# Kernel optimization log

Measured on AMD Instinct MI355X. Metric: run time of the kernel, lower is better.

The kernel has to match this reference:

```python
import jax, jax.numpy as jnp
import numpy as np

NODE_DIM = 64  # Net.node_dim


def _peg_conv(x, pos, edge_index, W, b, em_w, em_b):
    """PEGConv: GCN norm (with self-loops) + positional edge gate sigmoid(Linear(1,1)(sqdist))."""
    n = x.shape[0]
    loop = jnp.arange(n)
    row = jnp.concatenate([edge_index[0], loop])  # source j (with self-loops)
    col = jnp.concatenate([edge_index[1], loop])  # target i
    ones = jnp.ones(row.shape[0], dtype=x.dtype)
    deg = jax.ops.segment_sum(ones, col, num_segments=n)
    dinv = jnp.where(deg > 0, jax.lax.rsqrt(deg), 0.0)
    norm = dinv[row] * dinv[col]                                       # [E+N]
    h = x @ W                                                          # [N, out]
    sq = jnp.sum((pos[col] - pos[row]) ** 2, axis=-1, keepdims=True)   # [E+N, 1]
    gate = jax.nn.sigmoid(sq * em_w[0, 0] + em_b[0])                   # edge MLP Linear(1,1)+Sigmoid
    msg = gate * (norm[:, None] * h[row])                              # [E+N, out]
    return jax.ops.segment_sum(msg, col, num_segments=n) + b


def setup_inputs() -> dict:
    key = jax.random.key(0)
    ks = jax.random.split(key, 12)
    N, E_MP, E_LP = 50000, 800000, 100000
    IN, POS, HID = 128, 32, 64
    return {
        "x": jax.random.normal(ks[0], (N, IN), jnp.float32),
        "pos": jax.random.normal(ks[1], (N, POS), jnp.float32),
        "pos_edge_index": jax.random.randint(ks[2], (2, E_LP), 0, N),
        "neg_edge_index": jax.random.randint(ks[3], (2, E_LP), 0, N),
        "train_pos": jax.random.randint(ks[4], (2, E_MP), 0, N),
        "W1": jax.random.normal(ks[5], (IN, HID), jnp.float32) / np.float32(np.sqrt(IN)),
        "b1": jnp.zeros((HID,), jnp.float32),
        "em1_w": jax.random.normal(ks[6], (1, 1), jnp.float32),
        "em1_b": jnp.zeros((1,), jnp.float32),
        "W2": jax.random.normal(ks[7], (HID, HID), jnp.float32) / np.float32(np.sqrt(HID)),
        "b2": jnp.zeros((HID,), jnp.float32),
        "em2_w": jax.random.normal(ks[8], (1, 1), jnp.float32),
        "em2_b": jnp.zeros((1,), jnp.float32),
        "fc_w": jax.random.normal(ks[9], (1, 2), jnp.float32),  # nn.Linear(2,1) weight
        "fc_b": jnp.zeros((1,), jnp.float32),
    }


def reference(x, pos, pos_edge_index, neg_edge_index, train_pos,
              W1, b1, em1_w, em1_b, W2, b2, em2_w, em2_b, fc_w, fc_b):
    edge_index = jnp.concatenate([pos_edge_index, neg_edge_index], axis=-1)  # [2, 2*E_LP]
    h = _peg_conv(x, pos, train_pos, W1, b1, em1_w, em1_b)
    h = _peg_conv(h, pos, train_pos, W2, b2, em2_w, em2_b)
    nodes_first = h[edge_index[0], :NODE_DIM]
    nodes_second = h[edge_index[1], :NODE_DIM]
    pe = jnp.sum((pos[edge_index[0]] - pos[edge_index[1]]) ** 2, axis=-1, keepdims=True)
    pred = jnp.sum(nodes_first * nodes_second, axis=-1, keepdims=True)
    feats = jnp.concatenate([pred, pe], axis=1)  # [2*E_LP, 2]
    return feats @ fc_w.T + fc_b                 # [2*E_LP, 1]
```

## Files before the change

kernel.cpp:

```cpp
#include <hip/hip_runtime.h>

#define HID 64
#define POS_DIM 32
#define IN_DIM 128

using short8 = __attribute__((ext_vector_type(8))) short;
using f32x4  = __attribute__((ext_vector_type(4))) float;

__device__ __forceinline__ float fsig(float v) {
    return 1.0f / (1.0f + __expf(-v));
}

__device__ __forceinline__ unsigned short f2bf(float f) {
    unsigned int u = __float_as_uint(f);
    u = u + 0x7FFFu + ((u >> 16) & 1u);
    return (unsigned short)(u >> 16);
}
__device__ __forceinline__ float bf2f(unsigned short s) {
    return __uint_as_float(((unsigned int)s) << 16);
}
__device__ __forceinline__ float2 bfpair(unsigned int u) {
    return make_float2(__uint_as_float(u << 16),
                       __uint_as_float(u & 0xFFFF0000u));
}
__device__ __forceinline__ unsigned int pack2bf(float a, float b) {
    return (unsigned int)f2bf(a) | ((unsigned int)f2bf(b) << 16);
}

__global__ __launch_bounds__(256) void k_pre(const int* __restrict__ tp,
                                             const float* __restrict__ pos,
                                             int* cnt, float* __restrict__ sq,
                                             int* __restrict__ rank, int E) {
    int lane = threadIdx.x & 63;
    int wid  = threadIdx.x >> 6;
    int sub  = lane >> 3;
    int j    = lane & 7;
    int e = (blockIdx.x * 4 + wid) * 8 + sub;
    if (e >= E) return;
    int row = tp[e];
    int col = tp[E + e];
    float4 a = ((const float4*)(pos + (size_t)row * POS_DIM))[j];
    float4 b = ((const float4*)(pos + (size_t)col * POS_DIM))[j];
    float dx = a.x - b.x, dy = a.y - b.y, dz = a.z - b.z, dw = a.w - b.w;
    float s = 0.0f;
    s = fmaf(dx, dx, s); s = fmaf(dy, dy, s);
    s = fmaf(dz, dz, s); s = fmaf(dw, dw, s);
    s += __shfl_xor(s, 1);
    s += __shfl_xor(s, 2);
    s += __shfl_xor(s, 4);
    if (j == 0) {
        sq[e] = s;
        rank[e] = atomicAdd(&cnt[col], 1);
    }
}

__global__ __launch_bounds__(256) void k_bsum(const int* __restrict__ cnt,
                                              int* __restrict__ bsum, int n) {
    int i = blockIdx.x * 256 + threadIdx.x;
    int v = (i < n) ? cnt[i] : 0;
    #pragma unroll
    for (int o = 32; o; o >>= 1) v += __shfl_down(v, o);
    __shared__ int w[4];
    int lane = threadIdx.x & 63, wid = threadIdx.x >> 6;
    if (lane == 0) w[wid] = v;
    __syncthreads();
    if (threadIdx.x == 0) bsum[blockIdx.x] = w[0] + w[1] + w[2] + w[3];
}

__global__ __launch_bounds__(256) void k_scan2(const int* __restrict__ cnt,
                                               const int* __restrict__ bsum,
                                               int* __restrict__ off,
                                               float* __restrict__ dinv,
                                               int n, int Etot) {
    __shared__ int s[256];
    __shared__ int wsum[4];
    int tid = threadIdx.x, bid = blockIdx.x;
    int p = 0;
    for (int t = tid; t < bid; t += 256) p += bsum[t];
    #pragma unroll
    for (int o = 32; o; o >>= 1) p += __shfl_down(p, o);
    int lane = tid & 63, wid = tid >> 6;
    if (lane == 0) wsum[wid] = p;
    __syncthreads();
    int bpre = wsum[0] + wsum[1] + wsum[2] + wsum[3];
    int i = bid * 256 + tid;
    int v = (i < n) ? cnt[i] : 0;
    s[tid] = v;
    __syncthreads();
    #pragma unroll
    for (int d = 1; d < 256; d <<= 1) {
        int t_ = (tid >= d) ? s[tid - d] : 0;
        __syncthreads();
        s[tid] += t_;
        __syncthreads();
    }
    if (i < n) {
        off[i]  = bpre + s[tid] - v;
        dinv[i] = rsqrtf((float)(v + 1));
    }
    if (i == 0) off[n] = Etot;
}

__global__ __launch_bounds__(256) void k_fill(const int* __restrict__ tp,
                                              const int* __restrict__ off,
                                              const int* __restrict__ rank,
                                              const float* __restrict__ sq,
                                              const float* __restrict__ dinv,
                                              const float* em1w, const float* em1b,
                                              const float* em2w, const float* em2b,
                                              int4* __restrict__ csr, int E) {
    int e = blockIdx.x * blockDim.x + threadIdx.x;
    if (e >= E) return;
    int row = tp[e];
    int col = tp[E + e];
    int slot = off[col] + rank[e];
    float nrm = dinv[row] * dinv[col];
    float s = sq[e];
    float c1 = fsig(s * em1w[0] + em1b[0]) * nrm;
    float c2 = fsig(s * em2w[0] + em2b[0]) * nrm;
    csr[slot] = make_int4(row, __float_as_int(c1), __float_as_int(c2), 0);
}

template<int K, bool IN_BF16>
__global__ __launch_bounds__(256) void k_gemm_mfma(const void* __restrict__ Xv,
                                                   const float* __restrict__ W,
                                                   unsigned short* __restrict__ H,
                                                   int n) {
    constexpr int RB   = K * 2;
    constexpr int CPR  = K / 8;
    __shared__ unsigned char lds[64 * RB * 2];
    unsigned char* As = lds;
    unsigned char* Bt = lds + 64 * RB;

    int tid  = threadIdx.x;
    int row0 = blockIdx.x * 64;

    for (int i = tid; i < 64 * CPR; i += 256) {
        int r  = i / CPR;
        int kb = i % CPR;
        uint4 val;
        if (row0 + r < n) {
            if (IN_BF16) {
                val = *(const uint4*)((const unsigned short*)Xv + (size_t)(row0 + r) * K + kb * 8);
            } else {
                const float* src = (const float*)Xv + (size_t)(row0 + r) * K + kb * 8;
                float4 f0 = ((const float4*)src)[0];
                float4 f1 = ((const float4*)src)[1];
                val.x = pack2bf(f0.x, f0.y); val.y = pack2bf(f0.z, f0.w);
                val.z = pack2bf(f1.x, f1.y); val.w = pack2bf(f1.z, f1.w);
            }
        } else {
            val = make_uint4(0, 0, 0, 0);
        }
        *(uint4*)(As + r * RB + ((kb ^ (r & 7)) << 4)) = val;
    }
    for (int i = tid; i < K * 16; i += 256) {
        int k  = i / 16;
        int c0 = (i % 16) * 4;
        float4 w = ((const float4*)W)[i];
        #pragma unroll
        for (int u = 0; u < 4; ++u) {
            int c = c0 + u;
            float vv = (u == 0) ? w.x : (u == 1) ? w.y : (u == 2) ? w.z : w.w;
            int byte = c * RB + ((((k * 2) >> 4) ^ (c & 7)) << 4) + ((k & 7) * 2);
            *(unsigned short*)(Bt + byte) = f2bf(vv);
        }
    }
    __syncthreads();

    int wv   = tid >> 6;
    int lane = tid & 63;
    int l15  = lane & 15;
    int g    = lane >> 4;

    f32x4 acc[4] = {{0,0,0,0},{0,0,0,0},{0,0,0,0},{0,0,0,0}};
    #pragma unroll
    for (int kk = 0; kk < K / 32; ++kk) {
        int kc = kk * 4 + g;
        int arow = wv * 16 + l15;
        short8 a = *(const short8*)(As + arow * RB + ((kc ^ (arow & 7)) << 4));
        #pragma unroll
        for (int cb = 0; cb < 4; ++cb) {
            int c = cb * 16 + l15;
            short8 b = *(const short8*)(Bt + c * RB + ((kc ^ (c & 7)) << 4));
            acc[cb] = __builtin_amdgcn_mfma_f32_16x16x32_bf16(a, b, acc[cb], 0, 0, 0);
        }
    }

    #pragma unroll
    for (int cb = 0; cb < 4; ++cb) {
        #pragma unroll
        for (int r = 0; r < 4; ++r) {
            int row = row0 + wv * 16 + g * 4 + r;
            if (row < n) H[(size_t)row * HID + cb * 16 + l15] = f2bf(acc[cb][r]);
        }
    }
}

template<bool BF16OUT>
__global__ __launch_bounds__(256) void k_agg(const int* __restrict__ off,
                                             const int4* __restrict__ csr,
                                             const unsigned short* __restrict__ h,
                                             const float* __restrict__ dinv,
                                             const float* __restrict__ bias,
                                             const float* emb,
                                             void* __restrict__ outv, int n,
                                             int layer) {
    int wid  = threadIdx.x >> 6;
    int lane = threadIdx.x & 63;
    int i = blockIdx.x * 4 + wid;
    if (i >= n) return;
    float di = dinv[i];
    float gself = fsig(emb[0]);
    float acc = bias[lane] + gself * di * di * bf2f(h[(size_t)i * HID + lane]);
    int s = off[i], s1 = off[i + 1];
    for (; s + 4 <= s1; s += 4) {
        int4 e0 = csr[s],     e1 = csr[s + 1];
        int4 e2 = csr[s + 2], e3 = csr[s + 3];
        float c0 = __int_as_float(layer ? e0.z : e0.y);
        float c1 = __int_as_float(layer ? e1.z : e1.y);
        float c2 = __int_as_float(layer ? e2.z : e2.y);
        float c3 = __int_as_float(layer ? e3.z : e3.y);
        float v0 = bf2f(h[(size_t)e0.x * HID + lane]);
        float v1 = bf2f(h[(size_t)e1.x * HID + lane]);
        float v2 = bf2f(h[(size_t)e2.x * HID + lane]);
        float v3 = bf2f(h[(size_t)e3.x * HID + lane]);
        acc = fmaf(c0, v0, acc); acc = fmaf(c1, v1, acc);
        acc = fmaf(c2, v2, acc); acc = fmaf(c3, v3, acc);
    }
    for (; s < s1; ++s) {
        int4 e0 = csr[s];
        acc = fmaf(__int_as_float(layer ? e0.z : e0.y),
                   bf2f(h[(size_t)e0.x * HID + lane]), acc);
    }
    if (BF16OUT) ((unsigned short*)outv)[(size_t)i * HID + lane] = f2bf(acc);
    else         ((float*)outv)[(size_t)i * HID + lane] = acc;
}

__global__ __launch_bounds__(256) void k_predict(const int* __restrict__ pei,
                                                 const int* __restrict__ nei,
                                                 const unsigned short* __restrict__ h,
                                                 const float* __restrict__ pos,
                                                 const float* fcw, const float* fcb,
                                                 float* __restrict__ out, int Elp) {
    int j = threadIdx.x & 7;
    int e = blockIdx.x * 32 + (threadIdx.x >> 3);
    if (e >= 2 * Elp) return;
    int src, dst;
    if (e < Elp) { src = pei[e];        dst = pei[Elp + e]; }
    else         { src = nei[e - Elp];  dst = nei[e];       }
    uint4 hs = ((const uint4*)(h + (size_t)src * HID))[j];
    uint4 hd = ((const uint4*)(h + (size_t)dst * HID))[j];
    float p = 0.0f;
    {
        float2 a, b;
        a = bfpair(hs.x); b = bfpair(hd.x);
        p = fmaf(a.x, b.x, p); p = fmaf(a.y, b.y, p);
        a = bfpair(hs.y); b = bfpair(hd.y);
        p = fmaf(a.x, b.x, p); p = fmaf(a.y, b.y, p);
        a = bfpair(hs.z); b = bfpair(hd.z);
        p = fmaf(a.x, b.x, p); p = fmaf(a.y, b.y, p);
        a = bfpair(hs.w); b = bfpair(hd.w);
        p = fmaf(a.x, b.x, p); p = fmaf(a.y, b.y, p);
    }
    float4 pa = ((const float4*)(pos + (size_t)src * POS_DIM))[j];
    float4 pb = ((const float4*)(pos + (size_t)dst * POS_DIM))[j];
    float dx = pa.x - pb.x, dy = pa.y - pb.y, dz = pa.z - pb.z, dw = pa.w - pb.w;
    float pe = 0.0f;
    pe = fmaf(dx, dx, pe); pe = fmaf(dy, dy, pe);
    pe = fmaf(dz, dz, pe); pe = fmaf(dw, dw, pe);
    p  += __shfl_xor(p, 1);  pe += __shfl_xor(pe, 1);
    p  += __shfl_xor(p, 2);  pe += __shfl_xor(pe, 2);
    p  += __shfl_xor(p, 4);  pe += __shfl_xor(pe, 4);
    if (j == 0) out[e] = fcw[0] * p + fcw[1] * pe + fcb[0];
}

static inline size_t align16(size_t v) { return (v + 15) & ~(size_t)15; }

extern "C" void kernel_launch(void* const* d_in, const int* in_sizes, int n_in,
                              void* d_out, int out_size, void* d_ws, size_t ws_size,
                              hipStream_t stream) {
    const float* x    = (const float*)d_in[0];
    const float* pos  = (const float*)d_in[1];
    const int*   pei  = (const int*)d_in[2];
    const int*   nei  = (const int*)d_in[3];
    const int*   tp   = (const int*)d_in[4];
    const float* W1   = (const float*)d_in[5];
    const float* b1   = (const float*)d_in[6];
    const float* em1w = (const float*)d_in[7];
    const float* em1b = (const float*)d_in[8];
    const float* W2   = (const float*)d_in[9];
    const float* b2   = (const float*)d_in[10];
    const float* em2w = (const float*)d_in[11];
    const float* em2b = (const float*)d_in[12];
    const float* fcw  = (const float*)d_in[13];
    const float* fcb  = (const float*)d_in[14];
    float* outp = (float*)d_out;

    const int N   = in_sizes[0] / IN_DIM;
    const int E   = in_sizes[4] / 2;
    const int Elp = in_sizes[2] / 2;
    const int NB  = (N + 255) / 256;

    char* base = (char*)d_ws;
    size_t o = 0;
    int4* csr = (int4*)(base + o);          o += align16((size_t)E * 16);
    int*   cnt  = (int*)(base + o);         o += align16((size_t)N * 4);
    int*   off  = (int*)(base + o);         o += align16((size_t)(N + 1) * 4);
    int*   bsum = (int*)(base + o);         o += align16((size_t)NB * 4);
    float* dinv = (float*)(base + o);       o += align16((size_t)N * 4);
    unsigned short* obuf = (unsigned short*)(base + o); o += align16((size_t)N * HID * 4);
    char*  region = base + o;
    int*   rank = (int*)region;
    float* sq   = (float*)(region + align16((size_t)E * 4));
    unsigned short* hbuf = (unsigned short*)region;

    hipMemsetAsync(cnt, 0, (size_t)N * 4, stream);
    k_pre<<<(E + 31) / 32, 256, 0, stream>>>(tp, pos, cnt, sq, rank, E);
    k_bsum<<<NB, 256, 0, stream>>>(cnt, bsum, N);
    k_scan2<<<NB, 256, 0, stream>>>(cnt, bsum, off, dinv, N, E);
    k_fill<<<(E + 255) / 256, 256, 0, stream>>>(tp, off, rank, sq, dinv,
                                                em1w, em1b, em2w, em2b, csr, E);

    k_gemm_mfma<IN_DIM, false><<<(N + 63) / 64, 256, 0, stream>>>(x, W1, hbuf, N);
    k_agg<true><<<(N + 3) / 4, 256, 0, stream>>>(off, csr, hbuf, dinv, b1, em1b,
                                                 (void*)obuf, N, 0);

    k_gemm_mfma<HID, true><<<(N + 63) / 64, 256, 0, stream>>>(obuf, W2, hbuf, N);
    k_agg<true><<<(N + 3) / 4, 256, 0, stream>>>(off, csr, hbuf, dinv, b2, em2b,
                                                 (void*)obuf, N, 1);

    k_predict<<<(2 * Elp + 31) / 32, 256, 0, stream>>>(pei, nei, obuf,
                                                       pos, fcw, fcb, outp, Elp);
}
```

Baseline: 189.9 us.

## Restructure CSR build with cursor atomics and split aggregation across half-waves

The CSR build now runs a plain histogram kernel, then the scan also writes a per-node cursor array. A fused fill kernel computes the squared distance, gates and slot (via atomicAdd on the cursor) in one pass, which removes the rank and sq intermediate arrays and their extra global traffic. The aggregation kernel now has each half-wave process alternate edges, loading two packed bf16 features per lane, and combines the halves with a shuffle. This doubles edge-level parallelism per wavefront. The CSR order within a row becomes nondeterministic, so the float summation order varies between runs.

```diff
diff --git a/kernel.cpp b/kernel.cpp
--- a/kernel.cpp
+++ b/kernel.cpp
@@ -27,10 +27,69 @@
     return (unsigned int)f2bf(a) | ((unsigned int)f2bf(b) << 16);
 }
 
-__global__ __launch_bounds__(256) void k_pre(const int* __restrict__ tp,
-                                             const float* __restrict__ pos,
-                                             int* cnt, float* __restrict__ sq,
-                                             int* __restrict__ rank, int E) {
+__global__ __launch_bounds__(256) void k_hist(const int* __restrict__ tp,
+                                              int* cnt, int E) {
+    int i = blockIdx.x * blockDim.x + threadIdx.x;
+    if (i < E) atomicAdd(&cnt[tp[E + i]], 1);
+}
+
+__global__ __launch_bounds__(256) void k_bsum(const int* __restrict__ cnt,
+                                              int* __restrict__ bsum, int n) {
+    int i = blockIdx.x * 256 + threadIdx.x;
+    int v = (i < n) ? cnt[i] : 0;
+    #pragma unroll
+    for (int o = 32; o; o >>= 1) v += __shfl_down(v, o);
+    __shared__ int w[4];
+    int lane = threadIdx.x & 63, wid = threadIdx.x >> 6;
+    if (lane == 0) w[wid] = v;
+    __syncthreads();
+    if (threadIdx.x == 0) bsum[blockIdx.x] = w[0] + w[1] + w[2] + w[3];
+}
+
+__global__ __launch_bounds__(256) void k_scan2(const int* __restrict__ cnt,
+                                               const int* __restrict__ bsum,
+                                               int* __restrict__ off,
+                                               int* __restrict__ cur,
+                                               float* __restrict__ dinv,
+                                               int n, int Etot) {
+    __shared__ int s[256];
+    __shared__ int wsum[4];
+    int tid = threadIdx.x, bid = blockIdx.x;
+    int p = 0;
+    for (int t = tid; t < bid; t += 256) p += bsum[t];
+    #pragma unroll
+    for (int o = 32; o; o >>= 1) p += __shfl_down(p, o);
+    int lane = tid & 63, wid = tid >> 6;
+    if (lane == 0) wsum[wid] = p;
+    __syncthreads();
+    int bpre = wsum[0] + wsum[1] + wsum[2] + wsum[3];
+    int i = bid * 256 + tid;
+    int v = (i < n) ? cnt[i] : 0;
+    s[tid] = v;
+    __syncthreads();
+    #pragma unroll
+    for (int d = 1; d < 256; d <<= 1) {
+        int t_ = (tid >= d) ? s[tid - d] : 0;
+        __syncthreads();
+        s[tid] += t_;
+        __syncthreads();
+    }
+    if (i < n) {
+        int ov = bpre + s[tid] - v;
+        off[i]  = ov;
+        cur[i]  = ov;
+        dinv[i] = rsqrtf((float)(v + 1));
+    }
+    if (i == 0) off[n] = Etot;
+}
+
+__global__ __launch_bounds__(256) void k_fill2(const int* __restrict__ tp,
+                                               const float* __restrict__ pos,
+                                               const float* __restrict__ dinv,
+                                               int* cur,
+                                               const float* em1w, const float* em1b,
+                                               const float* em2w, const float* em2b,
+                                               int4* __restrict__ csr, int E) {
     int lane = threadIdx.x & 63;
     int wid  = threadIdx.x >> 6;
     int sub  = lane >> 3;
@@ -49,76 +108,12 @@
     s += __shfl_xor(s, 2);
     s += __shfl_xor(s, 4);
     if (j == 0) {
-        sq[e] = s;
-        rank[e] = atomicAdd(&cnt[col], 1);
-    }
-}
-
-__global__ __launch_bounds__(256) void k_bsum(const int* __restrict__ cnt,
-                                              int* __restrict__ bsum, int n) {
-    int i = blockIdx.x * 256 + threadIdx.x;
-    int v = (i < n) ? cnt[i] : 0;
-    #pragma unroll
-    for (int o = 32; o; o >>= 1) v += __shfl_down(v, o);
-    __shared__ int w[4];
-    int lane = threadIdx.x & 63, wid = threadIdx.x >> 6;
-    if (lane == 0) w[wid] = v;
-    __syncthreads();
-    if (threadIdx.x == 0) bsum[blockIdx.x] = w[0] + w[1] + w[2] + w[3];
-}
-
-__global__ __launch_bounds__(256) void k_scan2(const int* __restrict__ cnt,
-                                               const int* __restrict__ bsum,
-                                               int* __restrict__ off,
-                                               float* __restrict__ dinv,
-                                               int n, int Etot) {
-    __shared__ int s[256];
-    __shared__ int wsum[4];
-    int tid = threadIdx.x, bid = blockIdx.x;
-    int p = 0;
-    for (int t = tid; t < bid; t += 256) p += bsum[t];
-    #pragma unroll
-    for (int o = 32; o; o >>= 1) p += __shfl_down(p, o);
-    int lane = tid & 63, wid = tid >> 6;
-    if (lane == 0) wsum[wid] = p;
-    __syncthreads();
-    int bpre = wsum[0] + wsum[1] + wsum[2] + wsum[3];
-    int i = bid * 256 + tid;
-    int v = (i < n) ? cnt[i] : 0;
-    s[tid] = v;
-    __syncthreads();
-    #pragma unroll
-    for (int d = 1; d < 256; d <<= 1) {
-        int t_ = (tid >= d) ? s[tid - d] : 0;
-        __syncthreads();
-        s[tid] += t_;
-        __syncthreads();
-    }
-    if (i < n) {
-        off[i]  = bpre + s[tid] - v;
-        dinv[i] = rsqrtf((float)(v + 1));
-    }
-    if (i == 0) off[n] = Etot;
-}
-
-__global__ __launch_bounds__(256) void k_fill(const int* __restrict__ tp,
-                                              const int* __restrict__ off,
-                                              const int* __restrict__ rank,
-                                              const float* __restrict__ sq,
-                                              const float* __restrict__ dinv,
-                                              const float* em1w, const float* em1b,
-                                              const float* em2w, const float* em2b,
-                                              int4* __restrict__ csr, int E) {
-    int e = blockIdx.x * blockDim.x + threadIdx.x;
-    if (e >= E) return;
-    int row = tp[e];
-    int col = tp[E + e];
-    int slot = off[col] + rank[e];
-    float nrm = dinv[row] * dinv[col];
-    float s = sq[e];
-    float c1 = fsig(s * em1w[0] + em1b[0]) * nrm;
-    float c2 = fsig(s * em2w[0] + em2b[0]) * nrm;
-    csr[slot] = make_int4(row, __float_as_int(c1), __float_as_int(c2), 0);
+        float nrm = dinv[row] * dinv[col];
+        float c1 = fsig(s * em1w[0] + em1b[0]) * nrm;
+        float c2 = fsig(s * em2w[0] + em2b[0]) * nrm;
+        int slot = atomicAdd(&cur[col], 1);
+        csr[slot] = make_int4(row, __float_as_int(c1), __float_as_int(c2), 0);
+    }
 }
 
 template<int K, bool IN_BF16>
@@ -197,44 +192,51 @@
     }
 }
 
-template<bool BF16OUT>
 __global__ __launch_bounds__(256) void k_agg(const int* __restrict__ off,
                                              const int4* __restrict__ csr,
                                              const unsigned short* __restrict__ h,
                                              const float* __restrict__ dinv,
                                              const float* __restrict__ bias,
                                              const float* emb,
-                                             void* __restrict__ outv, int n,
-                                             int layer) {
+                                             unsigned short* __restrict__ out,
+                                             int n, int layer) {
     int wid  = threadIdx.x >> 6;
     int lane = threadIdx.x & 63;
+    int half = lane >> 5;
+    int q    = lane & 31;
     int i = blockIdx.x * 4 + wid;
     if (i >= n) return;
-    float di = dinv[i];
-    float gself = fsig(emb[0]);
-    float acc = bias[lane] + gself * di * di * bf2f(h[(size_t)i * HID + lane]);
-    int s = off[i], s1 = off[i + 1];
-    for (; s + 4 <= s1; s += 4) {
-        int4 e0 = csr[s],     e1 = csr[s + 1];
-        int4 e2 = csr[s + 2], e3 = csr[s + 3];
-        float c0 = __int_as_float(layer ? e0.z : e0.y);
-        float c1 = __int_as_float(layer ? e1.z : e1.y);
-        float c2 = __int_as_float(layer ? e2.z : e2.y);
-        float c3 = __int_as_float(layer ? e3.z : e3.y);
-        float v0 = bf2f(h[(size_t)e0.x * HID + lane]);
-        float v1 = bf2f(h[(size_t)e1.x * HID + lane]);
-        float v2 = bf2f(h[(size_t)e2.x * HID + lane]);
-        float v3 = bf2f(h[(size_t)e3.x * HID + lane]);
-        acc = fmaf(c0, v0, acc); acc = fmaf(c1, v1, acc);
-        acc = fmaf(c2, v2, acc); acc = fmaf(c3, v3, acc);
-    }
-    for (; s < s1; ++s) {
-        int4 e0 = csr[s];
-        acc = fmaf(__int_as_float(layer ? e0.z : e0.y),
-                   bf2f(h[(size_t)e0.x * HID + lane]), acc);
-    }
-    if (BF16OUT) ((unsigned short*)outv)[(size_t)i * HID + lane] = f2bf(acc);
-    else         ((float*)outv)[(size_t)i * HID + lane] = acc;
+    float accx = 0.0f, accy = 0.0f;
+    if (half == 0) {
+        float di = dinv[i];
+        float sc = fsig(emb[0]) * di * di;
+        float2 bv = ((const float2*)bias)[q];
+        float2 hv = bfpair(((const unsigned int*)(h + (size_t)i * HID))[q]);
+        accx = fmaf(sc, hv.x, bv.x);
+        accy = fmaf(sc, hv.y, bv.y);
+    }
+    int s  = off[i] + half;
+    int s1 = off[i + 1];
+    for (; s + 2 < s1; s += 4) {
+        int4 ea = csr[s];
+        int4 eb = csr[s + 2];
+        float ca = __int_as_float(layer ? ea.z : ea.y);
+        float cb = __int_as_float(layer ? eb.z : eb.y);
+        float2 va = bfpair(((const unsigned int*)(h + (size_t)ea.x * HID))[q]);
+        float2 vb = bfpair(((const unsigned int*)(h + (size_t)eb.x * HID))[q]);
+        accx = fmaf(ca, va.x, accx); accy = fmaf(ca, va.y, accy);
+        accx = fmaf(cb, vb.x, accx); accy = fmaf(cb, vb.y, accy);
+    }
+    if (s < s1) {
+        int4 ea = csr[s];
+        float ca = __int_as_float(layer ? ea.z : ea.y);
+        float2 va = bfpair(((const unsigned int*)(h + (size_t)ea.x * HID))[q]);
+        accx = fmaf(ca, va.x, accx); accy = fmaf(ca, va.y, accy);
+    }
+    accx += __shfl_down(accx, 32);
+    accy += __shfl_down(accy, 32);
+    if (half == 0)
+        ((unsigned int*)out)[(size_t)i * (HID / 2) + q] = pack2bf(accx, accy);
 }
 
 __global__ __launch_bounds__(256) void k_predict(const int* __restrict__ pei,
@@ -304,31 +306,27 @@
 
     char* base = (char*)d_ws;
     size_t o = 0;
-    int4* csr = (int4*)(base + o);          o += align16((size_t)E * 16);
-    int*   cnt  = (int*)(base + o);         o += align16((size_t)N * 4);
-    int*   off  = (int*)(base + o);         o += align16((size_t)(N + 1) * 4);
-    int*   bsum = (int*)(base + o);         o += align16((size_t)NB * 4);
-    float* dinv = (float*)(base + o);       o += align16((size_t)N * 4);
-    unsigned short* obuf = (unsigned short*)(base + o); o += align16((size_t)N * HID * 4);
-    char*  region = base + o;
-    int*   rank = (int*)region;
-    float* sq   = (float*)(region + align16((size_t)E * 4));
-    unsigned short* hbuf = (unsigned short*)region;
+    int4* csr = (int4*)(base + o);                        o += align16((size_t)E * 16);
+    int*   cnt  = (int*)(base + o);                       o += align16((size_t)N * 4);
+    int*   off  = (int*)(base + o);                       o += align16((size_t)(N + 1) * 4);
+    int*   cur  = (int*)(base + o);                       o += align16((size_t)N * 4);
+    int*   bsum = (int*)(base + o);                       o += align16((size_t)NB * 4);
+    float* dinv = (float*)(base + o);                     o += align16((size_t)N * 4);
+    unsigned short* hbuf = (unsigned short*)(base + o);   o += align16((size_t)N * HID * 2);
+    unsigned short* obuf = (unsigned short*)(base + o);   o += align16((size_t)N * HID * 2);
 
     hipMemsetAsync(cnt, 0, (size_t)N * 4, stream);
-    k_pre<<<(E + 31) / 32, 256, 0, stream>>>(tp, pos, cnt, sq, rank, E);
+    k_hist<<<(E + 255) / 256, 256, 0, stream>>>(tp, cnt, E);
     k_bsum<<<NB, 256, 0, stream>>>(cnt, bsum, N);
-    k_scan2<<<NB, 256, 0, stream>>>(cnt, bsum, off, dinv, N, E);
-    k_fill<<<(E + 255) / 256, 256, 0, stream>>>(tp, off, rank, sq, dinv,
-                                                em1w, em1b, em2w, em2b, csr, E);
+    k_scan2<<<NB, 256, 0, stream>>>(cnt, bsum, off, cur, dinv, N, E);
+    k_fill2<<<(E + 31) / 32, 256, 0, stream>>>(tp, pos, dinv, cur,
+                                               em1w, em1b, em2w, em2b, csr, E);
 
     k_gemm_mfma<IN_DIM, false><<<(N + 63) / 64, 256, 0, stream>>>(x, W1, hbuf, N);
-    k_agg<true><<<(N + 3) / 4, 256, 0, stream>>>(off, csr, hbuf, dinv, b1, em1b,
-                                                 (void*)obuf, N, 0);
+    k_agg<<<(N + 3) / 4, 256, 0, stream>>>(off, csr, hbuf, dinv, b1, em1b, obuf, N, 0);
 
     k_gemm_mfma<HID, true><<<(N + 63) / 64, 256, 0, stream>>>(obuf, W2, hbuf, N);
-    k_agg<true><<<(N + 3) / 4, 256, 0, stream>>>(off, csr, hbuf, dinv, b2, em2b,
-                                                 (void*)obuf, N, 1);
+    k_agg<<<(N + 3) / 4, 256, 0, stream>>>(off, csr, hbuf, dinv, b2, em2b, obuf, N, 1);
 
     k_predict<<<(2 * Elp + 31) / 32, 256, 0, stream>>>(pei, nei, obuf,
                                                        pos, fcw, fcb, outp, Elp);
```

Measured after the change: 200.3 us. 5.5% more time.
